# Kernel optimization log

Measured on AMD Instinct MI355X. Metric: run time of the kernel, lower is better.

Reference implementation:

```python
import jax, jax.numpy as jnp
import numpy as np

N_NODES = 20000
N_EDGES = 50000
IN_DIM = 128
HID = 128
OUT_DIM = 64
N_PAIRS = 128
N_LAYERS = 2
N_HEADS = 4


def setup_inputs() -> dict:
    key = jax.random.key(0)
    ks = jax.random.split(key, 32)
    s = 0.05
    def p(k, shape):
        return jax.random.normal(k, shape, jnp.float32) * s
    inp = {}
    inp["node_features"] = jax.random.normal(ks[0], (N_NODES, IN_DIM), jnp.float32)
    inp["edge_index"] = jax.random.randint(ks[1], (2, N_EDGES), 0, N_NODES, jnp.int32)
    inp["edge_timestamps"] = jax.random.uniform(ks[2], (N_EDGES,), jnp.float32)
    inp["target_pairs"] = jax.random.randint(ks[3], (N_PAIRS, 2), 0, N_NODES, jnp.int32)
    inp["in_W"] = p(ks[4], (HID, IN_DIM)); inp["in_b"] = p(ks[5], (HID,))
    inp["te_W1"] = p(ks[6], (N_LAYERS, HID, 1)); inp["te_b1"] = p(ks[7], (N_LAYERS, HID))
    inp["te_W2"] = p(ks[8], (N_LAYERS, HID, HID)); inp["te_b2"] = p(ks[9], (N_LAYERS, HID))
    inp["attn_in_W"] = p(ks[10], (N_LAYERS, 3 * HID, HID)); inp["attn_in_b"] = p(ks[11], (N_LAYERS, 3 * HID))
    inp["attn_out_W"] = p(ks[12], (N_LAYERS, HID, HID)); inp["attn_out_b"] = p(ks[13], (N_LAYERS, HID))
    inp["ft_W"] = p(ks[14], (N_LAYERS, HID, HID)); inp["ft_b"] = p(ks[15], (N_LAYERS, HID))
    inp["op_W"] = p(ks[16], (N_LAYERS, HID, HID)); inp["op_b"] = p(ks[17], (N_LAYERS, HID))
    inp["out1_W"] = p(ks[18], (HID, HID)); inp["out1_b"] = p(ks[19], (HID,))
    inp["out2_W"] = p(ks[20], (OUT_DIM, HID)); inp["out2_b"] = p(ks[21], (OUT_DIM,))
    inp["lp1_W"] = p(ks[22], (HID, 2 * OUT_DIM)); inp["lp1_b"] = p(ks[23], (HID,))
    inp["lp2_W"] = p(ks[24], (HID // 2, HID)); inp["lp2_b"] = p(ks[25], (HID // 2,))
    inp["lp3_W"] = p(ks[26], (1, HID // 2)); inp["lp3_b"] = p(ks[27], (1,))
    return inp


def _forward(node_features, edge_index, edge_timestamps, target_pairs,
             in_W, in_b, te_W1, te_b1, te_W2, te_b2,
             attn_in_W, attn_in_b, attn_out_W, attn_out_b,
             ft_W, ft_b, op_W, op_b,
             out1_W, out1_b, out2_W, out2_b,
             lp1_W, lp1_b, lp2_W, lp2_b, lp3_W, lp3_b):
    N = node_features.shape[0]
    h = in_W.shape[0]
    H = N_HEADS
    d = h // H
    scale = 1.0 / np.sqrt(d).astype(np.float32)
    src, dst = edge_index[0], edge_index[1]
    # flattened target nodes; duplicates compute identical rows so dedup (torch.unique) is unneeded
    targets = target_pairs.reshape(-1)  # [U]
    U = targets.shape[0]
    E = src.shape[0]

    x = node_features @ in_W.T + in_b  # [N, h]
    for l in range(te_W1.shape[0]):
        tf = x @ ft_W[l].T + ft_b[l]                                           # [N, h]
        tfeat = jax.nn.relu(edge_timestamps[:, None] @ te_W1[l].T + te_b1[l])
        tfeat = tfeat @ te_W2[l].T + te_b2[l]                                  # [E, h]
        Wq, Wk, Wv = jnp.split(attn_in_W[l], 3, axis=0)
        bq, bk, bv = jnp.split(attn_in_b[l], 3)
        q = (tf[targets] @ Wq.T + bq).reshape(U, H, d)
        # keys/values are linear in (tf[nbr] + tfeat): split into node term A and edge term B
        Ak = (tf @ Wk.T).reshape(N, H, d)
        Bk = (tfeat @ Wk.T + bk).reshape(E, H, d)
        Av = (tf @ Wv.T).reshape(N, H, d)
        Bv = (tfeat @ Wv.T + bv).reshape(E, H, d)
        is_src = src[None, :] == targets[:, None]          # [U, E]
        mask = is_src | (dst[None, :] == targets[:, None])  # edge incident to target
        nbr = jnp.where(is_src, dst[None, :], src[None, :])  # other endpoint, [U, E]
        qAk = jnp.einsum('uhd,nhd->uhn', q, Ak) * scale      # [U, H, N]
        idx = jnp.broadcast_to(nbr[:, None, :], (U, H, E))
        s_node = jnp.take_along_axis(qAk, idx, axis=2)        # [U, H, E]
        s_edge = jnp.einsum('uhd,ehd->uhe', q, Bk) * scale
        scores = jnp.where(mask[:, None, :], s_node + s_edge, -1e30)
        p = jax.nn.softmax(scores, axis=-1)
        p = jnp.where(mask[:, None, :], p, 0.0)               # [U, H, E]
        out_edge = jnp.einsum('uhe,ehd->uhd', p, Bv)
        # sum_e p * Av[nbr] via per-target scatter of probs into node space
        w = jax.vmap(lambda pe, ne: jax.ops.segment_sum(pe, ne, num_segments=N))(
            p.transpose(0, 2, 1), nbr)                        # [U, N, H]
        out_node = jnp.einsum('unh,nhd->uhd', w, Av)
        attn = (out_node + out_edge).reshape(U, h) @ attn_out_W[l].T + attn_out_b[l]
        has_nbr = mask.any(axis=1)
        agg_in = jnp.where(has_nbr[:, None], attn, tf[targets])
        agg = agg_in @ op_W[l].T + op_b[l]
        x = x.at[targets].set(agg)
        x = jax.nn.relu(x)
    emb = jax.nn.relu(x @ out1_W.T + out1_b) @ out2_W.T + out2_b  # [N, out]
    pair = jnp.concatenate([emb[target_pairs[:, 0]], emb[target_pairs[:, 1]]], axis=1)
    z = jax.nn.relu(pair @ lp1_W.T + lp1_b)
    z = jax.nn.relu(z @ lp2_W.T + lp2_b)
    return jax.nn.sigmoid(z @ lp3_W.T + lp3_b)  # [B, 1]


def reference(node_features, edge_index, edge_timestamps, target_pairs,
              in_W, in_b, te_W1, te_b1, te_W2, te_b2,
              attn_in_W, attn_in_b, attn_out_W, attn_out_b,
              ft_W, ft_b, op_W, op_b,
              out1_W, out1_b, out2_W, out2_b,
              lp1_W, lp1_b, lp2_W, lp2_b, lp3_W, lp3_b):
    return _forward(node_features, edge_index, edge_timestamps, target_pairs,
                    in_W, in_b, te_W1, te_b1, te_W2, te_b2,
                    attn_in_W, attn_in_b, attn_out_W, attn_out_b,
                    ft_W, ft_b, op_W, op_b,
                    out1_W, out1_b, out2_W, out2_b,
                    lp1_W, lp1_b, lp2_W, lp2_b, lp3_W, lp3_b)
```

## Files before the change

kernel.cpp:

```cpp
#include <hip/hip_runtime.h>
#include <math.h>

#define N_NODES 20000
#define N_EDGES 50000
#define N_SLOTS 256
#define N_PAIRS 128
#define CAP 64
#define MSTRIDE 16384
#define NMAT 19
#define TFLAG (1 << 30)

__device__ __forceinline__ float4 relu4(float4 v) {
    return make_float4(fmaxf(v.x, 0.f), fmaxf(v.y, 0.f), fmaxf(v.z, 0.f), fmaxf(v.w, 0.f));
}
__device__ __forceinline__ float4 add4(float4 a, float4 b) {
    return make_float4(a.x + b.x, a.y + b.y, a.z + b.z, a.w + b.w);
}
__device__ __forceinline__ void fma4(float4& acc, const float4 w, const float s) {
    acc.x = fmaf(w.x, s, acc.x); acc.y = fmaf(w.y, s, acc.y);
    acc.z = fmaf(w.z, s, acc.z); acc.w = fmaf(w.w, s, acc.w);
}
#define F4Z make_float4(0.f, 0.f, 0.f, 0.f)

__device__ __forceinline__ float4 mv_ks1_g8(const float* __restrict__ WT,
                                            const float* __restrict__ xv128,
                                            int g, int jj) {
    const float4* W4 = (const float4*)WT;
    const float4* x4 = (const float4*)xv128;
    float4 acc = F4Z;
#pragma unroll
    for (int kk4 = 0; kk4 < 4; ++kk4) {
        int k4 = g * 4 + kk4;
        float4 xv = x4[k4];
        fma4(acc, W4[(k4 * 4 + 0) * 32 + jj], xv.x);
        fma4(acc, W4[(k4 * 4 + 1) * 32 + jj], xv.y);
        fma4(acc, W4[(k4 * 4 + 2) * 32 + jj], xv.z);
        fma4(acc, W4[(k4 * 4 + 3) * 32 + jj], xv.w);
    }
    return acc;
}
__device__ __forceinline__ float4 mv_ks1_g8_64(const float* __restrict__ WT,
                                               const float* __restrict__ xv128,
                                               int g, int jj) {
    const float4* W4 = (const float4*)WT;
    const float4* x4 = (const float4*)xv128;
    int j16 = jj & 15;
    float4 acc = F4Z;
#pragma unroll
    for (int kk4 = 0; kk4 < 4; ++kk4) {
        int k4 = g * 4 + kk4;
        float4 xv = x4[k4];
        fma4(acc, W4[(k4 * 4 + 0) * 16 + j16], xv.x);
        fma4(acc, W4[(k4 * 4 + 1) * 16 + j16], xv.y);
        fma4(acc, W4[(k4 * 4 + 2) * 16 + j16], xv.z);
        fma4(acc, W4[(k4 * 4 + 3) * 16 + j16], xv.w);
    }
    return acc;
}
__device__ __forceinline__ void mv8_g8(const float* __restrict__ WT,
                                       const float* __restrict__ xs,
                                       int g, int jj, float4* acc) {
    const float4* W4 = (const float4*)WT;
    const float4* x4 = (const float4*)xs;
#pragma unroll
    for (int kk4 = 0; kk4 < 4; ++kk4) {
        int k4 = g * 4 + kk4;
        float4 w0 = W4[(k4 * 4 + 0) * 32 + jj];
        float4 w1 = W4[(k4 * 4 + 1) * 32 + jj];
        float4 w2 = W4[(k4 * 4 + 2) * 32 + jj];
        float4 w3 = W4[(k4 * 4 + 3) * 32 + jj];
#pragma unroll
        for (int e = 0; e < 8; ++e) {
            float4 xv = x4[e * 32 + k4];
            fma4(acc[e], w0, xv.x); fma4(acc[e], w1, xv.y);
            fma4(acc[e], w2, xv.z); fma4(acc[e], w3, xv.w);
        }
    }
}
__device__ __forceinline__ float4 comb1_g8(const float4* pb, int jj) {
    float4 s = pb[jj];
#pragma unroll
    for (int gp = 1; gp < 8; ++gp) s = add4(s, pb[gp * 32 + jj]);
    return s;
}
__device__ __forceinline__ float4 comb8_g8(const float4* pb, int it, int jj) {
    float4 s = pb[it * 32 + jj];
#pragma unroll
    for (int gp = 1; gp < 8; ++gp) s = add4(s, pb[(gp * 8 + it) * 32 + jj]);
    return s;
}

__device__ __forceinline__ float4 mv_ks1(const float* __restrict__ WT,
                                         const float* __restrict__ xv128,
                                         int g, int jj) {
    const float4* W4 = (const float4*)WT;
    const float4* x4 = (const float4*)xv128;
    float4 acc = F4Z;
#pragma unroll 2
    for (int kk4 = 0; kk4 < 8; ++kk4) {
        int k4 = g * 8 + kk4;
        float4 xv = x4[k4];
        fma4(acc, W4[(k4 * 4 + 0) * 32 + jj], xv.x);
        fma4(acc, W4[(k4 * 4 + 1) * 32 + jj], xv.y);
        fma4(acc, W4[(k4 * 4 + 2) * 32 + jj], xv.z);
        fma4(acc, W4[(k4 * 4 + 3) * 32 + jj], xv.w);
    }
    return acc;
}
__device__ __forceinline__ float4 mv_ks1_64(const float* __restrict__ WT,
                                            const float* __restrict__ xv128,
                                            int g, int jj) {
    const float4* W4 = (const float4*)WT;
    const float4* x4 = (const float4*)xv128;
    int j16 = jj & 15;
    float4 acc = F4Z;
#pragma unroll 2
    for (int kk4 = 0; kk4 < 8; ++kk4) {
        int k4 = g * 8 + kk4;
        float4 xv = x4[k4];
        fma4(acc, W4[(k4 * 4 + 0) * 16 + j16], xv.x);
        fma4(acc, W4[(k4 * 4 + 1) * 16 + j16], xv.y);
        fma4(acc, W4[(k4 * 4 + 2) * 16 + j16], xv.z);
        fma4(acc, W4[(k4 * 4 + 3) * 16 + j16], xv.w);
    }
    return acc;
}
__device__ __forceinline__ float4 comb1(const float4* pb, int jj) {
    return add4(add4(pb[jj], pb[32 + jj]), add4(pb[64 + jj], pb[96 + jj]));
}


__global__ __launch_bounds__(256) void k_prep_tr(
    const int* __restrict__ ei, const int* __restrict__ tp,
    const float* __restrict__ inW, const float* __restrict__ ftW,
    const float* __restrict__ teW2, const float* __restrict__ aiW,
    const float* __restrict__ aoW, const float* __restrict__ opW,
    const float* __restrict__ o1W, const float* __restrict__ o2W,
    const float* __restrict__ l1W, const float* __restrict__ l2W,
    float* __restrict__ WT, int* __restrict__ cnt, int2* __restrict__ lst) {
    __shared__ float tile[32][129];
    __shared__ int tps[N_SLOTS];
    __shared__ int lc;
    const int b = blockIdx.x;
    if (threadIdx.x == 0) lc = 0;
    if (b < 72) {
        int m, r0, rows;
        if (b < 68) { m = b >> 2; r0 = (b & 3) * 32; rows = 128; }
        else { int mm = b - 68; m = 17 + (mm >> 1); r0 = (mm & 1) * 32; rows = 64; }
        const float* src;
        if (m == 0) src = inW;
        else if (m <= 2) src = ftW + (m - 1) * MSTRIDE;
        else if (m <= 4) src = teW2 + (m - 3) * MSTRIDE;
        else if (m <= 10) src = aiW + (m - 5) * MSTRIDE;
        else if (m <= 12) src = aoW + (m - 11) * MSTRIDE;
        else if (m <= 14) src = opW + (m - 13) * MSTRIDE;
        else if (m == 15) src = o1W;
        else if (m == 16) src = l1W;
        else if (m == 17) src = o2W;
        else src = l2W;
        float* dst = WT + m * MSTRIDE;
        for (int idx = threadIdx.x; idx < 32 * 128; idx += 256) {
            int r = idx >> 7, c = idx & 127;
            tile[r][c] = src[(r0 + r) * 128 + c];
        }
        __syncthreads();
        for (int idx = threadIdx.x; idx < 128 * 32; idx += 256) {
            int k = idx >> 5, jr = idx & 31;
            dst[k * rows + r0 + jr] = tile[jr][k];
        }
    }
    for (int i = threadIdx.x; i < N_SLOTS; i += 256) tps[i] = tp[i];
    __syncthreads();
    const int u = tps[b];
    const int4* src4 = (const int4*)ei;
    const int4* dst4 = (const int4*)(ei + N_EDGES);
    for (int e4 = threadIdx.x; e4 < N_EDGES / 4; e4 += 256) {
        int4 s = src4[e4];
        int4 d = dst4[e4];
        int ss[4] = {s.x, s.y, s.z, s.w};
        int dd[4] = {d.x, d.y, d.z, d.w};
#pragma unroll
        for (int t = 0; t < 4; ++t) {
            if (ss[t] == u || dd[t] == u) {
                int nbr = (ss[t] == u) ? dd[t] : ss[t];
                int pos = atomicAdd(&lc, 1);
                if (pos < CAP) lst[b * CAP + pos] = make_int2(e4 * 4 + t, nbr);
            }
        }
    }
    __syncthreads();
    if (threadIdx.x == 0) cnt[b] = lc;
    int c = min(lc, CAP);
    if (threadIdx.x < c) {
        int2 en = lst[b * CAP + threadIdx.x];
        bool ist = false;
        for (int t = 0; t < N_SLOTS; ++t) ist |= (tps[t] == en.y);
        if (ist) { en.y |= TFLAG; lst[b * CAP + threadIdx.x] = en; }
    }
}

__global__ __launch_bounds__(256) void k_layer(
    const float* __restrict__ nf, const float* __restrict__ x,
    const float* __restrict__ ts, const int* __restrict__ tp,
    const int* __restrict__ cnt, const int2* __restrict__ lst,
    const float* __restrict__ WT_in, const float* __restrict__ inb,
    const float* __restrict__ WT_ft, const float* __restrict__ ftb,
    const float* __restrict__ teW1, const float* __restrict__ teb1,
    const float* __restrict__ WT_te2, const float* __restrict__ teb2,
    const float* __restrict__ WT_q, const float* __restrict__ bq,
    const float* __restrict__ WT_k, const float* __restrict__ bk,
    const float* __restrict__ WT_v, const float* __restrict__ bv,
    const float* __restrict__ WT_ao, const float* __restrict__ aob,
    const float* __restrict__ WT_op, const float* __restrict__ opb,
    const float* __restrict__ WT_o1, const float* __restrict__ o1b,
    const float* __restrict__ WT_o2, const float* __restrict__ o2b,
    float* __restrict__ x_out, float* __restrict__ emb, int layer) {
    __shared__ __align__(16) float xu[128], x0u[128], tfv[128], qv[128], sv[128];
    __shared__ __align__(16) float xs[8 * 128], t1s[8 * 128], x0s[8 * 128], zs[8 * 128];
    __shared__ __align__(16) float4 pb[8 * 8 * 32];
    __shared__ __align__(16) float vbl[CAP * 128];
    __shared__ float scl[CAP * 4];
    __shared__ int nbr_s[8], tf_s[8];
    __shared__ float ts_s[8];
    const int slot = blockIdx.x, tid = threadIdx.x, g = tid >> 5, jj = tid & 31;
    const float scale = 0.17677669529663687f;
    const int u = tp[slot];
    const int c = min(cnt[slot], CAP);

    if (tid < 128) xu[tid] = (layer == 0) ? nf[(size_t)u * 128 + tid]
                                          : x[(size_t)u * 128 + tid];
    __syncthreads();
    const float* xeff = xu;
    if (layer == 0) {
        pb[g * 32 + jj] = mv_ks1_g8(WT_in, xu, g, jj);
        __syncthreads();
        if (g == 0)
            *(float4*)(x0u + jj * 4) = add4(comb1_g8(pb, jj), *(const float4*)(inb + jj * 4));
        xeff = x0u;
        __syncthreads();
    }
    pb[g * 32 + jj] = mv_ks1_g8(WT_ft, xeff, g, jj);
    __syncthreads();
    if (g == 0)
        *(float4*)(tfv + jj * 4) = add4(comb1_g8(pb, jj), *(const float4*)(ftb + jj * 4));
    __syncthreads();
    pb[g * 32 + jj] = mv_ks1_g8(WT_q, tfv, g, jj);
    __syncthreads();
    if (g == 0)
        *(float4*)(qv + jj * 4) = add4(comb1_g8(pb, jj), *(const float4*)(bq + jj * 4));
    __syncthreads();

    for (int base = 0; base < c; base += 8) {
        if (tid < 8) {
            int i = base + tid;
            int2 en = (i < c) ? lst[slot * CAP + i] : make_int2(0, 0);
            nbr_s[tid] = en.y & ~TFLAG;
            tf_s[tid] = (en.y & TFLAG) ? 1 : 0;
            ts_s[tid] = (i < c) ? ts[en.x] : 0.f;
        }
        __syncthreads();
        {
            int e = tid >> 5, c0 = jj * 4;
            const float* srcp = (layer == 0) ? (nf + (size_t)nbr_s[e] * 128 + c0)
                                             : (x + (size_t)nbr_s[e] * 128 + c0);
            float4 v = *(const float4*)srcp;
            float* dstp = (layer == 0) ? xs : x0s;
            *(float4*)(dstp + e * 128 + c0) = v;
            float tse = ts_s[e];
            float4 w = *(const float4*)(teW1 + c0);
            float4 b = *(const float4*)(teb1 + c0);
            *(float4*)(t1s + e * 128 + c0) =
                make_float4(fmaxf(fmaf(tse, w.x, b.x), 0.f),
                            fmaxf(fmaf(tse, w.y, b.y), 0.f),
                            fmaxf(fmaf(tse, w.z, b.z), 0.f),
                            fmaxf(fmaf(tse, w.w, b.w), 0.f));
        }
        __syncthreads();
        if (layer == 0) {
            float4 acc[8] = {F4Z, F4Z, F4Z, F4Z, F4Z, F4Z, F4Z, F4Z};
            mv8_g8(WT_in, xs, g, jj, acc);
#pragma unroll
            for (int e = 0; e < 8; ++e) pb[(g * 8 + e) * 32 + jj] = acc[e];
            __syncthreads();
            {
                float4 x0v = add4(comb8_g8(pb, g, jj), *(const float4*)(inb + jj * 4));
                *(float4*)(x0s + g * 128 + jj * 4) = x0v;
                if (base + g < c && !tf_s[g])
                    *(float4*)(x_out + (size_t)nbr_s[g] * 128 + jj * 4) = relu4(x0v);
            }
            __syncthreads();
        }
        {
            float4 acc[8] = {F4Z, F4Z, F4Z, F4Z, F4Z, F4Z, F4Z, F4Z};
            mv8_g8(WT_ft, x0s, g, jj, acc);
#pragma unroll
            for (int e = 0; e < 8; ++e) pb[(g * 8 + e) * 32 + jj] = acc[e];
            __syncthreads();
            float4 za = comb8_g8(pb, g, jj);
            __syncthreads();
            float4 acc2[8] = {F4Z, F4Z, F4Z, F4Z, F4Z, F4Z, F4Z, F4Z};
            mv8_g8(WT_te2, t1s, g, jj, acc2);
#pragma unroll
            for (int e = 0; e < 8; ++e) pb[(g * 8 + e) * 32 + jj] = acc2[e];
            __syncthreads();
            float4 zb = comb8_g8(pb, g, jj);
            float4 z4 = add4(add4(za, zb),
                             add4(*(const float4*)(ftb + jj * 4),
                                  *(const float4*)(teb2 + jj * 4)));
            *(float4*)(zs + g * 128 + jj * 4) = z4;
            __syncthreads();
        }
        {
            float4 acc[8] = {F4Z, F4Z, F4Z, F4Z, F4Z, F4Z, F4Z, F4Z};
            mv8_g8(WT_k, zs, g, jj, acc);
#pragma unroll
            for (int e = 0; e < 8; ++e) pb[(g * 8 + e) * 32 + jj] = acc[e];
            __syncthreads();
            float4 kk = add4(comb8_g8(pb, g, jj), *(const float4*)(bk + jj * 4));
            __syncthreads();
            float4 acc2[8] = {F4Z, F4Z, F4Z, F4Z, F4Z, F4Z, F4Z, F4Z};
            mv8_g8(WT_v, zs, g, jj, acc2);
#pragma unroll
            for (int e = 0; e < 8; ++e) pb[(g * 8 + e) * 32 + jj] = acc2[e];
            __syncthreads();
            float4 vv = add4(comb8_g8(pb, g, jj), *(const float4*)(bv + jj * 4));
            float4 q4 = *(const float4*)(qv + jj * 4);
            float pr = q4.x * kk.x + q4.y * kk.y + q4.z * kk.z + q4.w * kk.w;
            pr += __shfl_xor(pr, 1);
            pr += __shfl_xor(pr, 2);
            pr += __shfl_xor(pr, 4);
            if (base + g < c) {
                if ((jj & 7) == 0) scl[(base + g) * 4 + (jj >> 3)] = pr * scale;
                *(float4*)(vbl + (base + g) * 128 + jj * 4) = vv;
            }
            __syncthreads();
        }
    }

    if (tid < 128) {
        int h = tid >> 5;
        if (c > 0) {
            float m = -INFINITY;
            for (int i = 0; i < c; ++i) m = fmaxf(m, scl[i * 4 + h]);
            float l = 0.f, o = 0.f;
            for (int i = 0; i < c; ++i) {
                float p = __expf(scl[i * 4 + h] - m);
                l += p;
                o = fmaf(p, vbl[i * 128 + tid], o);
            }
            sv[tid] = o / l;
        } else {
            sv[tid] = 0.f;
        }
    }
    __syncthreads();
    pb[g * 32 + jj] = mv_ks1_g8(WT_ao, sv, g, jj);
    __syncthreads();
    if (g == 0) {
        float4 z4;
        if (c > 0) z4 = add4(comb1_g8(pb, jj), *(const float4*)(aob + jj * 4));
        else z4 = *(const float4*)(tfv + jj * 4);
        *(float4*)(xu + jj * 4) = z4;
    }
    __syncthreads();
    pb[g * 32 + jj] = mv_ks1_g8(WT_op, xu, g, jj);
    __syncthreads();
    if (layer == 0) {
        if (g == 0) {
            float4 a = relu4(add4(comb1_g8(pb, jj), *(const float4*)(opb + jj * 4)));
            *(float4*)(x_out + (size_t)u * 128 + jj * 4) = a;
        }
        return;
    }
    if (g == 0)
        *(float4*)(x0u + jj * 4) =
            relu4(add4(comb1_g8(pb, jj), *(const float4*)(opb + jj * 4)));
    __syncthreads();
    pb[g * 32 + jj] = mv_ks1_g8(WT_o1, x0u, g, jj);
    __syncthreads();
    if (g == 0)
        *(float4*)(tfv + jj * 4) =
            relu4(add4(comb1_g8(pb, jj), *(const float4*)(o1b + jj * 4)));
    __syncthreads();
    pb[g * 32 + jj] = mv_ks1_g8_64(WT_o2, tfv, g, jj);
    __syncthreads();
    if (g == 0 && jj < 16)
        *(float4*)(emb + (size_t)slot * 64 + jj * 4) =
            add4(comb1_g8(pb, jj), *(const float4*)(o2b + jj * 4));
}

__global__ __launch_bounds__(128) void k_pair(
    const float* __restrict__ emb,
    const float* __restrict__ WT_l1, const float* __restrict__ l1b,
    const float* __restrict__ WT_l2, const float* __restrict__ l2b,
    const float* __restrict__ l3W, const float* __restrict__ l3b,
    float* __restrict__ out) {
    __shared__ __align__(16) float pv[128], z1[128], z2s[64];
    __shared__ __align__(16) float4 pb[4 * 32];
    const int p = blockIdx.x, tid = threadIdx.x, g = tid >> 5, jj = tid & 31;
    pv[tid] = (tid < 64) ? emb[(size_t)(2 * p) * 64 + tid]
                         : emb[(size_t)(2 * p + 1) * 64 + (tid - 64)];
    __syncthreads();
    pb[g * 32 + jj] = mv_ks1(WT_l1, pv, g, jj);
    __syncthreads();
    if (g == 0)
        *(float4*)(z1 + jj * 4) = relu4(add4(comb1(pb, jj), *(const float4*)(l1b + jj * 4)));
    __syncthreads();
    pb[g * 32 + jj] = mv_ks1_64(WT_l2, z1, g, jj);
    __syncthreads();
    if (g == 0 && jj < 16)
        *(float4*)(z2s + jj * 4) = relu4(add4(comb1(pb, jj), *(const float4*)(l2b + jj * 4)));
    __syncthreads();
    if (tid < 64) {
        float v = z2s[tid] * l3W[tid];
        v += __shfl_xor(v, 1);
        v += __shfl_xor(v, 2);
        v += __shfl_xor(v, 4);
        v += __shfl_xor(v, 8);
        v += __shfl_xor(v, 16);
        v += __shfl_xor(v, 32);
        if (tid == 0) out[p] = 1.f / (1.f + __expf(-(v + l3b[0])));
    }
}

extern "C" void kernel_launch(void* const* d_in, const int* in_sizes, int n_in,
                              void* d_out, int out_size, void* d_ws, size_t ws_size,
                              hipStream_t stream) {
    const float* nf  = (const float*)d_in[0];
    const int*   ei  = (const int*)d_in[1];
    const float* ts  = (const float*)d_in[2];
    const int*   tp  = (const int*)d_in[3];
    const float* inW = (const float*)d_in[4];
    const float* inb = (const float*)d_in[5];
    const float* teW1 = (const float*)d_in[6];
    const float* teb1 = (const float*)d_in[7];
    const float* teW2 = (const float*)d_in[8];
    const float* teb2 = (const float*)d_in[9];
    const float* aiW = (const float*)d_in[10];
    const float* aib = (const float*)d_in[11];
    const float* aoW = (const float*)d_in[12];
    const float* aob = (const float*)d_in[13];
    const float* ftW = (const float*)d_in[14];
    const float* ftb = (const float*)d_in[15];
    const float* opW = (const float*)d_in[16];
    const float* opb = (const float*)d_in[17];
    const float* o1W = (const float*)d_in[18];
    const float* o1b = (const float*)d_in[19];
    const float* o2W = (const float*)d_in[20];
    const float* o2b = (const float*)d_in[21];
    const float* l1W = (const float*)d_in[22];
    const float* l1b = (const float*)d_in[23];
    const float* l2W = (const float*)d_in[24];
    const float* l2b = (const float*)d_in[25];
    const float* l3W = (const float*)d_in[26];
    const float* l3b = (const float*)d_in[27];
    float* out = (float*)d_out;

    char* ws = (char*)d_ws;
    size_t off = 0;
    float* x    = (float*)(ws + off); off += (size_t)N_NODES * 128 * 4;
    int*   cnt  = (int*)  (ws + off); off += N_SLOTS * 4;
    int2*  lst  = (int2*) (ws + off); off += (size_t)N_SLOTS * CAP * 8;
    float* emb  = (float*)(ws + off); off += N_SLOTS * 64 * 4;
    float* WT   = (float*)(ws + off); off += (size_t)NMAT * MSTRIDE * 4;

    k_prep_tr<<<N_SLOTS, 256, 0, stream>>>(ei, tp, inW, ftW, teW2, aiW, aoW, opW,
                                           o1W, o2W, l1W, l2W, WT, cnt, lst);

    for (int l = 0; l < 2; ++l) {
        const float* WT_ft = WT + (1 + l) * MSTRIDE;
        const float* WT_te2 = WT + (3 + l) * MSTRIDE;
        const float* WT_q = WT + (5 + 3 * l) * MSTRIDE;
        const float* WT_k = WT + (6 + 3 * l) * MSTRIDE;
        const float* WT_v = WT + (7 + 3 * l) * MSTRIDE;
        const float* WT_ao = WT + (11 + l) * MSTRIDE;
        const float* WT_op = WT + (13 + l) * MSTRIDE;
        const float* bq = aib + l * 384;
        k_layer<<<N_SLOTS, 256, 0, stream>>>(
            nf, x, ts, tp, cnt, lst,
            WT, inb, WT_ft, ftb + l * 128, teW1 + l * 128, teb1 + l * 128,
            WT_te2, teb2 + l * 128, WT_q, bq, WT_k, bq + 128, WT_v, bq + 256,
            WT_ao, aob + l * 128, WT_op, opb + l * 128,
            WT + 15 * MSTRIDE, o1b, WT + 17 * MSTRIDE, o2b,
            x, emb, l);
    }
    k_pair<<<N_PAIRS, 128, 0, stream>>>(emb, WT + 16 * MSTRIDE, l1b,
                                        WT + 18 * MSTRIDE, l2b, l3W, l3b, out);
}
```

Measured before the change: 200.9 us.

## Precompose Q/K/V with feature-transform weights and fuse pair head into last layer

Precomputes products of the attention Q/K/V projection matrices with the feature-transform and time-encoding weights, plus folded biases, in the prep kernel. The layer kernel then goes from input to q, k and v in one matvec stage, and the K and V matvecs share a single barrier. The separate pair-MLP kernel is removed: the second block of each pair finishes it, detected through an atomic counter and threadfence. This cuts sequential matvec stages, barriers and one launch, at the cost of more prep work, doubled shared staging, and different float rounding from reassociation.

```diff
diff --git a/kernel.cpp b/kernel.cpp
--- a/kernel.cpp
+++ b/kernel.cpp
@@ -8,6 +8,7 @@
 #define CAP 64
 #define MSTRIDE 16384
 #define NMAT 19
+#define NPROD 10
 #define TFLAG (1 << 30)
 
 __device__ __forceinline__ float4 relu4(float4 v) {
@@ -90,59 +91,29 @@
     return s;
 }
 
-__device__ __forceinline__ float4 mv_ks1(const float* __restrict__ WT,
-                                         const float* __restrict__ xv128,
-                                         int g, int jj) {
-    const float4* W4 = (const float4*)WT;
-    const float4* x4 = (const float4*)xv128;
-    float4 acc = F4Z;
-#pragma unroll 2
-    for (int kk4 = 0; kk4 < 8; ++kk4) {
-        int k4 = g * 8 + kk4;
-        float4 xv = x4[k4];
-        fma4(acc, W4[(k4 * 4 + 0) * 32 + jj], xv.x);
-        fma4(acc, W4[(k4 * 4 + 1) * 32 + jj], xv.y);
-        fma4(acc, W4[(k4 * 4 + 2) * 32 + jj], xv.z);
-        fma4(acc, W4[(k4 * 4 + 3) * 32 + jj], xv.w);
-    }
-    return acc;
-}
-__device__ __forceinline__ float4 mv_ks1_64(const float* __restrict__ WT,
-                                            const float* __restrict__ xv128,
-                                            int g, int jj) {
-    const float4* W4 = (const float4*)WT;
-    const float4* x4 = (const float4*)xv128;
-    int j16 = jj & 15;
-    float4 acc = F4Z;
-#pragma unroll 2
-    for (int kk4 = 0; kk4 < 8; ++kk4) {
-        int k4 = g * 8 + kk4;
-        float4 xv = x4[k4];
-        fma4(acc, W4[(k4 * 4 + 0) * 16 + j16], xv.x);
-        fma4(acc, W4[(k4 * 4 + 1) * 16 + j16], xv.y);
-        fma4(acc, W4[(k4 * 4 + 2) * 16 + j16], xv.z);
-        fma4(acc, W4[(k4 * 4 + 3) * 16 + j16], xv.w);
-    }
-    return acc;
-}
-__device__ __forceinline__ float4 comb1(const float4* pb, int jj) {
-    return add4(add4(pb[jj], pb[32 + jj]), add4(pb[64 + jj], pb[96 + jj]));
-}
-
 
 __global__ __launch_bounds__(256) void k_prep_tr(
     const int* __restrict__ ei, const int* __restrict__ tp,
     const float* __restrict__ inW, const float* __restrict__ ftW,
     const float* __restrict__ teW2, const float* __restrict__ aiW,
+    const float* __restrict__ aib,
     const float* __restrict__ aoW, const float* __restrict__ opW,
     const float* __restrict__ o1W, const float* __restrict__ o2W,
     const float* __restrict__ l1W, const float* __restrict__ l2W,
-    float* __restrict__ WT, int* __restrict__ cnt, int2* __restrict__ lst) {
+    const float* __restrict__ ftb, const float* __restrict__ teb2,
+    float* __restrict__ WT, float* __restrict__ WP, float* __restrict__ WB,
+    int* __restrict__ pairflag,
+    int* __restrict__ cnt, int2* __restrict__ lst) {
     __shared__ float tile[32][129];
+    __shared__ __align__(16) float As[128 * 128];
+    __shared__ __align__(16) float Bs[128 * 16];
+    __shared__ float bv_s[128];
     __shared__ int tps[N_SLOTS];
     __shared__ int lc;
     const int b = blockIdx.x;
-    if (threadIdx.x == 0) lc = 0;
+    const int tid = threadIdx.x;
+    if (tid == 0) lc = 0;
+    if (b == 0 && tid < N_PAIRS) pairflag[tid] = 0;
     if (b < 72) {
         int m, r0, rows;
         if (b < 68) { m = b >> 2; r0 = (b & 3) * 32; rows = 128; }
@@ -159,43 +130,100 @@
         else if (m == 17) src = o2W;
         else src = l2W;
         float* dst = WT + m * MSTRIDE;
-        for (int idx = threadIdx.x; idx < 32 * 128; idx += 256) {
+        for (int idx = tid; idx < 32 * 128; idx += 256) {
             int r = idx >> 7, c = idx & 127;
             tile[r][c] = src[(r0 + r) * 128 + c];
         }
         __syncthreads();
-        for (int idx = threadIdx.x; idx < 128 * 32; idx += 256) {
+        for (int idx = tid; idx < 128 * 32; idx += 256) {
             int k = idx >> 5, jr = idx & 31;
             dst[k * rows + r0 + jr] = tile[jr][k];
         }
-    }
-    for (int i = threadIdx.x; i < N_SLOTS; i += 256) tps[i] = tp[i];
+    } else if (b < 152) {
+        const int pidx = (b - 72) >> 3, mseg = (b - 72) & 7, m0 = mseg * 16;
+        const int l = pidx / 5, t = pidx % 5;
+        const float* A = aiW + l * 3 * MSTRIDE +
+                         ((t == 0) ? 0 : (t <= 2) ? MSTRIDE : 2 * MSTRIDE);
+        const float* B = ((t == 2 || t == 4) ? teW2 : ftW) + l * MSTRIDE;
+        {
+            const float4* A4 = (const float4*)A;
+            float4* As4 = (float4*)As;
+            for (int idx = tid; idx < 4096; idx += 256) As4[idx] = A4[idx];
+            for (int idx = tid; idx < 2048; idx += 256) {
+                int j = idx >> 4, mm = idx & 15;
+                Bs[idx] = B[j * 128 + m0 + mm];
+            }
+            if (tid < 128) {
+                float bb = ftb[l * 128 + tid];
+                if (t != 0) bb += teb2[l * 128 + tid];
+                bv_s[tid] = bb;
+            }
+        }
+        __syncthreads();
+        {
+            const int i = tid & 127, half = tid >> 7;
+            const float4* As4 = (const float4*)As;
+            const float4* Bs4 = (const float4*)Bs;
+            float4 accA = F4Z, accB = F4Z;
+#pragma unroll 4
+            for (int j4 = 0; j4 < 32; ++j4) {
+                float4 a4 = As4[i * 32 + j4];
+#pragma unroll
+                for (int jo = 0; jo < 4; ++jo) {
+                    int j = j4 * 4 + jo;
+                    float aj = (jo == 0) ? a4.x : (jo == 1) ? a4.y : (jo == 2) ? a4.z : a4.w;
+                    float4 b0 = Bs4[j * 4 + half * 2 + 0];
+                    float4 b1 = Bs4[j * 4 + half * 2 + 1];
+                    fma4(accA, b0, aj);
+                    fma4(accB, b1, aj);
+                }
+            }
+            float* dst = WP + pidx * MSTRIDE;
+            float o[8] = {accA.x, accA.y, accA.z, accA.w, accB.x, accB.y, accB.z, accB.w};
+#pragma unroll
+            for (int r = 0; r < 8; ++r) dst[(m0 + half * 8 + r) * 128 + i] = o[r];
+        }
+        if (mseg == 0 && (t == 0 || t == 1 || t == 3) && tid < 128) {
+            const float4* As4 = (const float4*)As;
+            const float4* bs4 = (const float4*)bv_s;
+            float acc = 0.f;
+#pragma unroll 4
+            for (int j4 = 0; j4 < 32; ++j4) {
+                float4 a4 = As4[tid * 32 + j4];
+                float4 b4 = bs4[j4];
+                acc = fmaf(a4.x, b4.x, fmaf(a4.y, b4.y, fmaf(a4.z, b4.z, fmaf(a4.w, b4.w, acc))));
+            }
+            int which = (t == 0) ? 0 : (t == 1) ? 1 : 2;
+            WB[l * 384 + which * 128 + tid] = acc + aib[l * 384 + which * 128 + tid];
+        }
+    }
+    for (int i = tid; i < N_SLOTS; i += 256) tps[i] = tp[i];
     __syncthreads();
     const int u = tps[b];
     const int4* src4 = (const int4*)ei;
     const int4* dst4 = (const int4*)(ei + N_EDGES);
-    for (int e4 = threadIdx.x; e4 < N_EDGES / 4; e4 += 256) {
+    for (int e4 = tid; e4 < N_EDGES / 4; e4 += 256) {
         int4 s = src4[e4];
         int4 d = dst4[e4];
         int ss[4] = {s.x, s.y, s.z, s.w};
         int dd[4] = {d.x, d.y, d.z, d.w};
 #pragma unroll
-        for (int t = 0; t < 4; ++t) {
-            if (ss[t] == u || dd[t] == u) {
-                int nbr = (ss[t] == u) ? dd[t] : ss[t];
+        for (int t2 = 0; t2 < 4; ++t2) {
+            if (ss[t2] == u || dd[t2] == u) {
+                int nbr = (ss[t2] == u) ? dd[t2] : ss[t2];
                 int pos = atomicAdd(&lc, 1);
-                if (pos < CAP) lst[b * CAP + pos] = make_int2(e4 * 4 + t, nbr);
-            }
-        }
-    }
-    __syncthreads();
-    if (threadIdx.x == 0) cnt[b] = lc;
+                if (pos < CAP) lst[b * CAP + pos] = make_int2(e4 * 4 + t2, nbr);
+            }
+        }
+    }
+    __syncthreads();
+    if (tid == 0) cnt[b] = lc;
     int c = min(lc, CAP);
-    if (threadIdx.x < c) {
-        int2 en = lst[b * CAP + threadIdx.x];
+    if (tid < c) {
+        int2 en = lst[b * CAP + tid];
         bool ist = false;
-        for (int t = 0; t < N_SLOTS; ++t) ist |= (tps[t] == en.y);
-        if (ist) { en.y |= TFLAG; lst[b * CAP + threadIdx.x] = en; }
+        for (int t2 = 0; t2 < N_SLOTS; ++t2) ist |= (tps[t2] == en.y);
+        if (ist) { en.y |= TFLAG; lst[b * CAP + tid] = en; }
     }
 }
 
@@ -206,26 +234,33 @@
     const float* __restrict__ WT_in, const float* __restrict__ inb,
     const float* __restrict__ WT_ft, const float* __restrict__ ftb,
     const float* __restrict__ teW1, const float* __restrict__ teb1,
-    const float* __restrict__ WT_te2, const float* __restrict__ teb2,
-    const float* __restrict__ WT_q, const float* __restrict__ bq,
-    const float* __restrict__ WT_k, const float* __restrict__ bk,
-    const float* __restrict__ WT_v, const float* __restrict__ bv,
+    const float* __restrict__ WPq, const float* __restrict__ WkF,
+    const float* __restrict__ WkT, const float* __restrict__ WvF,
+    const float* __restrict__ WvT, const float* __restrict__ WBl,
     const float* __restrict__ WT_ao, const float* __restrict__ aob,
     const float* __restrict__ WT_op, const float* __restrict__ opb,
     const float* __restrict__ WT_o1, const float* __restrict__ o1b,
     const float* __restrict__ WT_o2, const float* __restrict__ o2b,
-    float* __restrict__ x_out, float* __restrict__ emb, int layer) {
+    const float* __restrict__ WT_l1, const float* __restrict__ l1b,
+    const float* __restrict__ WT_l2, const float* __restrict__ l2b,
+    const float* __restrict__ l3W, const float* __restrict__ l3b,
+    float* __restrict__ x_out, float* __restrict__ emb,
+    int* __restrict__ pairflag, float* __restrict__ out, int layer) {
     __shared__ __align__(16) float xu[128], x0u[128], tfv[128], qv[128], sv[128];
-    __shared__ __align__(16) float xs[8 * 128], t1s[8 * 128], x0s[8 * 128], zs[8 * 128];
-    __shared__ __align__(16) float4 pb[8 * 8 * 32];
+    __shared__ __align__(16) float xs[8 * 128], t1s[8 * 128], x0s[8 * 128];
+    __shared__ __align__(16) float4 pb[2 * 8 * 8 * 32];
     __shared__ __align__(16) float vbl[CAP * 128];
     __shared__ float scl[CAP * 4];
     __shared__ int nbr_s[8], tf_s[8];
     __shared__ float ts_s[8];
+    __shared__ int win_s;
     const int slot = blockIdx.x, tid = threadIdx.x, g = tid >> 5, jj = tid & 31;
     const float scale = 0.17677669529663687f;
     const int u = tp[slot];
     const int c = min(cnt[slot], CAP);
+    const float* bqp = WBl;
+    const float* bkp = WBl + 128;
+    const float* bvp = WBl + 256;
 
     if (tid < 128) xu[tid] = (layer == 0) ? nf[(size_t)u * 128 + tid]
                                           : x[(size_t)u * 128 + tid];
@@ -240,14 +275,12 @@
         __syncthreads();
     }
     pb[g * 32 + jj] = mv_ks1_g8(WT_ft, xeff, g, jj);
-    __syncthreads();
-    if (g == 0)
+    pb[2048 + g * 32 + jj] = mv_ks1_g8(WPq, xeff, g, jj);
+    __syncthreads();
+    if (g == 0) {
         *(float4*)(tfv + jj * 4) = add4(comb1_g8(pb, jj), *(const float4*)(ftb + jj * 4));
-    __syncthreads();
-    pb[g * 32 + jj] = mv_ks1_g8(WT_q, tfv, g, jj);
-    __syncthreads();
-    if (g == 0)
-        *(float4*)(qv + jj * 4) = add4(comb1_g8(pb, jj), *(const float4*)(bq + jj * 4));
+        *(float4*)(qv + jj * 4) = add4(comb1_g8(pb + 2048, jj), *(const float4*)(bqp + jj * 4));
+    }
     __syncthreads();
 
     for (int base = 0; base < c; base += 8) {
@@ -292,38 +325,18 @@
         }
         {
             float4 acc[8] = {F4Z, F4Z, F4Z, F4Z, F4Z, F4Z, F4Z, F4Z};
-            mv8_g8(WT_ft, x0s, g, jj, acc);
+            mv8_g8(WkF, x0s, g, jj, acc);
+            mv8_g8(WkT, t1s, g, jj, acc);
 #pragma unroll
             for (int e = 0; e < 8; ++e) pb[(g * 8 + e) * 32 + jj] = acc[e];
+            float4 acc2[8] = {F4Z, F4Z, F4Z, F4Z, F4Z, F4Z, F4Z, F4Z};
+            mv8_g8(WvF, x0s, g, jj, acc2);
+            mv8_g8(WvT, t1s, g, jj, acc2);
+#pragma unroll
+            for (int e = 0; e < 8; ++e) pb[2048 + (g * 8 + e) * 32 + jj] = acc2[e];
             __syncthreads();
-            float4 za = comb8_g8(pb, g, jj);
-            __syncthreads();
-            float4 acc2[8] = {F4Z, F4Z, F4Z, F4Z, F4Z, F4Z, F4Z, F4Z};
-            mv8_g8(WT_te2, t1s, g, jj, acc2);
-#pragma unroll
-            for (int e = 0; e < 8; ++e) pb[(g * 8 + e) * 32 + jj] = acc2[e];
-            __syncthreads();
-            float4 zb = comb8_g8(pb, g, jj);
-            float4 z4 = add4(add4(za, zb),
-                             add4(*(const float4*)(ftb + jj * 4),
-                                  *(const float4*)(teb2 + jj * 4)));
-            *(float4*)(zs + g * 128 + jj * 4) = z4;
-            __syncthreads();
-        }
-        {
-            float4 acc[8] = {F4Z, F4Z, F4Z, F4Z, F4Z, F4Z, F4Z, F4Z};
-            mv8_g8(WT_k, zs, g, jj, acc);
-#pragma unroll
-            for (int e = 0; e < 8; ++e) pb[(g * 8 + e) * 32 + jj] = acc[e];
-            __syncthreads();
-            float4 kk = add4(comb8_g8(pb, g, jj), *(const float4*)(bk + jj * 4));
-            __syncthreads();
-            float4 acc2[8] = {F4Z, F4Z, F4Z, F4Z, F4Z, F4Z, F4Z, F4Z};
-            mv8_g8(WT_v, zs, g, jj, acc2);
-#pragma unroll
-            for (int e = 0; e < 8; ++e) pb[(g * 8 + e) * 32 + jj] = acc2[e];
-            __syncthreads();
-            float4 vv = add4(comb8_g8(pb, g, jj), *(const float4*)(bv + jj * 4));
+            float4 kk = add4(comb8_g8(pb, g, jj), *(const float4*)(bkp + jj * 4));
+            float4 vv = add4(comb8_g8(pb + 2048, g, jj), *(const float4*)(bvp + jj * 4));
             float4 q4 = *(const float4*)(qv + jj * 4);
             float pr = q4.x * kk.x + q4.y * kk.y + q4.z * kk.z + q4.w * kk.w;
             pr += __shfl_xor(pr, 1);
@@ -384,35 +397,33 @@
     __syncthreads();
     pb[g * 32 + jj] = mv_ks1_g8_64(WT_o2, tfv, g, jj);
     __syncthreads();
-    if (g == 0 && jj < 16)
+    if (g == 0 && jj < 16) {
         *(float4*)(emb + (size_t)slot * 64 + jj * 4) =
             add4(comb1_g8(pb, jj), *(const float4*)(o2b + jj * 4));
-}
-
-__global__ __launch_bounds__(128) void k_pair(
-    const float* __restrict__ emb,
-    const float* __restrict__ WT_l1, const float* __restrict__ l1b,
-    const float* __restrict__ WT_l2, const float* __restrict__ l2b,
-    const float* __restrict__ l3W, const float* __restrict__ l3b,
-    float* __restrict__ out) {
-    __shared__ __align__(16) float pv[128], z1[128], z2s[64];
-    __shared__ __align__(16) float4 pb[4 * 32];
-    const int p = blockIdx.x, tid = threadIdx.x, g = tid >> 5, jj = tid & 31;
-    pv[tid] = (tid < 64) ? emb[(size_t)(2 * p) * 64 + tid]
-                         : emb[(size_t)(2 * p + 1) * 64 + (tid - 64)];
-    __syncthreads();
-    pb[g * 32 + jj] = mv_ks1(WT_l1, pv, g, jj);
+        __threadfence();
+    }
+    __syncthreads();
+    if (tid == 0) win_s = atomicAdd(&pairflag[slot >> 1], 1);
+    __syncthreads();
+    if (win_s == 0) return;
+    __threadfence();
+    const int p = slot >> 1;
+    if (tid < 128)
+        sv[tid] = (tid < 64) ? emb[(size_t)(2 * p) * 64 + tid]
+                             : emb[(size_t)(2 * p + 1) * 64 + (tid - 64)];
+    __syncthreads();
+    pb[g * 32 + jj] = mv_ks1_g8(WT_l1, sv, g, jj);
     __syncthreads();
     if (g == 0)
-        *(float4*)(z1 + jj * 4) = relu4(add4(comb1(pb, jj), *(const float4*)(l1b + jj * 4)));
-    __syncthreads();
-    pb[g * 32 + jj] = mv_ks1_64(WT_l2, z1, g, jj);
+        *(float4*)(xu + jj * 4) = relu4(add4(comb1_g8(pb, jj), *(const float4*)(l1b + jj * 4)));
+    __syncthreads();
+    pb[g * 32 + jj] = mv_ks1_g8_64(WT_l2, xu, g, jj);
     __syncthreads();
     if (g == 0 && jj < 16)
-        *(float4*)(z2s + jj * 4) = relu4(add4(comb1(pb, jj), *(const float4*)(l2b + jj * 4)));
+        *(float4*)(x0u + jj * 4) = relu4(add4(comb1_g8(pb, jj), *(const float4*)(l2b + jj * 4)));
     __syncthreads();
     if (tid < 64) {
-        float v = z2s[tid] * l3W[tid];
+        float v = x0u[tid] * l3W[tid];
         v += __shfl_xor(v, 1);
         v += __shfl_xor(v, 2);
         v += __shfl_xor(v, 4);
@@ -462,28 +473,31 @@
     int*   cnt  = (int*)  (ws + off); off += N_SLOTS * 4;
     int2*  lst  = (int2*) (ws + off); off += (size_t)N_SLOTS * CAP * 8;
     float* emb  = (float*)(ws + off); off += N_SLOTS * 64 * 4;
+    int*   pfl  = (int*)  (ws + off); off += N_PAIRS * 4;
     float* WT   = (float*)(ws + off); off += (size_t)NMAT * MSTRIDE * 4;
-
-    k_prep_tr<<<N_SLOTS, 256, 0, stream>>>(ei, tp, inW, ftW, teW2, aiW, aoW, opW,
-                                           o1W, o2W, l1W, l2W, WT, cnt, lst);
+    float* WP   = (float*)(ws + off); off += (size_t)NPROD * MSTRIDE * 4;
+    float* WB   = (float*)(ws + off); off += 2 * 384 * 4;
+
+    k_prep_tr<<<N_SLOTS, 256, 0, stream>>>(ei, tp, inW, ftW, teW2, aiW, aib,
+                                           aoW, opW, o1W, o2W, l1W, l2W,
+                                           ftb, teb2, WT, WP, WB, pfl, cnt, lst);
 
     for (int l = 0; l < 2; ++l) {
         const float* WT_ft = WT + (1 + l) * MSTRIDE;
-        const float* WT_te2 = WT + (3 + l) * MSTRIDE;
-        const float* WT_q = WT + (5 + 3 * l) * MSTRIDE;
-        const float* WT_k = WT + (6 + 3 * l) * MSTRIDE;
-        const float* WT_v = WT + (7 + 3 * l) * MSTRIDE;
+        const float* WPq = WP + (l * 5 + 0) * MSTRIDE;
+        const float* WkF = WP + (l * 5 + 1) * MSTRIDE;
+        const float* WkT = WP + (l * 5 + 2) * MSTRIDE;
+        const float* WvF = WP + (l * 5 + 3) * MSTRIDE;
+        const float* WvT = WP + (l * 5 + 4) * MSTRIDE;
         const float* WT_ao = WT + (11 + l) * MSTRIDE;
         const float* WT_op = WT + (13 + l) * MSTRIDE;
-        const float* bq = aib + l * 384;
         k_layer<<<N_SLOTS, 256, 0, stream>>>(
             nf, x, ts, tp, cnt, lst,
             WT, inb, WT_ft, ftb + l * 128, teW1 + l * 128, teb1 + l * 128,
-            WT_te2, teb2 + l * 128, WT_q, bq, WT_k, bq + 128, WT_v, bq + 256,
+            WPq, WkF, WkT, WvF, WvT, WB + l * 384,
             WT_ao, aob + l * 128, WT_op, opb + l * 128,
             WT + 15 * MSTRIDE, o1b, WT + 17 * MSTRIDE, o2b,
-            x, emb, l);
-    }
-    k_pair<<<N_PAIRS, 128, 0, stream>>>(emb, WT + 16 * MSTRIDE, l1b,
-                                        WT + 18 * MSTRIDE, l2b, l3W, l3b, out);
-}
+            WT + 16 * MSTRIDE, l1b, WT + 18 * MSTRIDE, l2b, l3W, l3b,
+            x, emb, pfl, out, l);
+    }
+}
```

New measurement: 345.9 us. 72.2% more time.

## Fuse pair-prediction MLP into final layer kernel via last-arriver atomic flag

Applied to the files above, without the earlier changes.

Drops the separate k_pair launch. Each block of the last layer publishes its embedding, bumps a per-pair atomic counter, and the second block of each pair to arrive runs the link-prediction MLP with the 8-group matvec helpers. This removes one kernel launch and its dependency gap. In exchange it adds threadfences and an atomic to every layer block, and relies on correct memory ordering for cross-block emb visibility.

```diff
diff --git a/kernel.cpp b/kernel.cpp
--- a/kernel.cpp
+++ b/kernel.cpp
@@ -90,45 +90,6 @@
     return s;
 }
 
-__device__ __forceinline__ float4 mv_ks1(const float* __restrict__ WT,
-                                         const float* __restrict__ xv128,
-                                         int g, int jj) {
-    const float4* W4 = (const float4*)WT;
-    const float4* x4 = (const float4*)xv128;
-    float4 acc = F4Z;
-#pragma unroll 2
-    for (int kk4 = 0; kk4 < 8; ++kk4) {
-        int k4 = g * 8 + kk4;
-        float4 xv = x4[k4];
-        fma4(acc, W4[(k4 * 4 + 0) * 32 + jj], xv.x);
-        fma4(acc, W4[(k4 * 4 + 1) * 32 + jj], xv.y);
-        fma4(acc, W4[(k4 * 4 + 2) * 32 + jj], xv.z);
-        fma4(acc, W4[(k4 * 4 + 3) * 32 + jj], xv.w);
-    }
-    return acc;
-}
-__device__ __forceinline__ float4 mv_ks1_64(const float* __restrict__ WT,
-                                            const float* __restrict__ xv128,
-                                            int g, int jj) {
-    const float4* W4 = (const float4*)WT;
-    const float4* x4 = (const float4*)xv128;
-    int j16 = jj & 15;
-    float4 acc = F4Z;
-#pragma unroll 2
-    for (int kk4 = 0; kk4 < 8; ++kk4) {
-        int k4 = g * 8 + kk4;
-        float4 xv = x4[k4];
-        fma4(acc, W4[(k4 * 4 + 0) * 16 + j16], xv.x);
-        fma4(acc, W4[(k4 * 4 + 1) * 16 + j16], xv.y);
-        fma4(acc, W4[(k4 * 4 + 2) * 16 + j16], xv.z);
-        fma4(acc, W4[(k4 * 4 + 3) * 16 + j16], xv.w);
-    }
-    return acc;
-}
-__device__ __forceinline__ float4 comb1(const float4* pb, int jj) {
-    return add4(add4(pb[jj], pb[32 + jj]), add4(pb[64 + jj], pb[96 + jj]));
-}
-
 
 __global__ __launch_bounds__(256) void k_prep_tr(
     const int* __restrict__ ei, const int* __restrict__ tp,
@@ -137,12 +98,14 @@
     const float* __restrict__ aoW, const float* __restrict__ opW,
     const float* __restrict__ o1W, const float* __restrict__ o2W,
     const float* __restrict__ l1W, const float* __restrict__ l2W,
-    float* __restrict__ WT, int* __restrict__ cnt, int2* __restrict__ lst) {
+    float* __restrict__ WT, int* __restrict__ pairflag,
+    int* __restrict__ cnt, int2* __restrict__ lst) {
     __shared__ float tile[32][129];
     __shared__ int tps[N_SLOTS];
     __shared__ int lc;
     const int b = blockIdx.x;
     if (threadIdx.x == 0) lc = 0;
+    if (b == 0 && threadIdx.x < N_PAIRS) pairflag[threadIdx.x] = 0;
     if (b < 72) {
         int m, r0, rows;
         if (b < 68) { m = b >> 2; r0 = (b & 3) * 32; rows = 128; }
@@ -214,7 +177,11 @@
     const float* __restrict__ WT_op, const float* __restrict__ opb,
     const float* __restrict__ WT_o1, const float* __restrict__ o1b,
     const float* __restrict__ WT_o2, const float* __restrict__ o2b,
-    float* __restrict__ x_out, float* __restrict__ emb, int layer) {
+    const float* __restrict__ WT_l1, const float* __restrict__ l1b,
+    const float* __restrict__ WT_l2, const float* __restrict__ l2b,
+    const float* __restrict__ l3W, const float* __restrict__ l3b,
+    float* __restrict__ x_out, float* __restrict__ emb,
+    int* __restrict__ pairflag, float* __restrict__ out, int layer) {
     __shared__ __align__(16) float xu[128], x0u[128], tfv[128], qv[128], sv[128];
     __shared__ __align__(16) float xs[8 * 128], t1s[8 * 128], x0s[8 * 128], zs[8 * 128];
     __shared__ __align__(16) float4 pb[8 * 8 * 32];
@@ -222,6 +189,7 @@
     __shared__ float scl[CAP * 4];
     __shared__ int nbr_s[8], tf_s[8];
     __shared__ float ts_s[8];
+    __shared__ int win_s;
     const int slot = blockIdx.x, tid = threadIdx.x, g = tid >> 5, jj = tid & 31;
     const float scale = 0.17677669529663687f;
     const int u = tp[slot];
@@ -384,35 +352,33 @@
     __syncthreads();
     pb[g * 32 + jj] = mv_ks1_g8_64(WT_o2, tfv, g, jj);
     __syncthreads();
-    if (g == 0 && jj < 16)
+    if (g == 0 && jj < 16) {
         *(float4*)(emb + (size_t)slot * 64 + jj * 4) =
             add4(comb1_g8(pb, jj), *(const float4*)(o2b + jj * 4));
-}
-
-__global__ __launch_bounds__(128) void k_pair(
-    const float* __restrict__ emb,
-    const float* __restrict__ WT_l1, const float* __restrict__ l1b,
-    const float* __restrict__ WT_l2, const float* __restrict__ l2b,
-    const float* __restrict__ l3W, const float* __restrict__ l3b,
-    float* __restrict__ out) {
-    __shared__ __align__(16) float pv[128], z1[128], z2s[64];
-    __shared__ __align__(16) float4 pb[4 * 32];
-    const int p = blockIdx.x, tid = threadIdx.x, g = tid >> 5, jj = tid & 31;
-    pv[tid] = (tid < 64) ? emb[(size_t)(2 * p) * 64 + tid]
-                         : emb[(size_t)(2 * p + 1) * 64 + (tid - 64)];
-    __syncthreads();
-    pb[g * 32 + jj] = mv_ks1(WT_l1, pv, g, jj);
+        __threadfence();
+    }
+    __syncthreads();
+    if (tid == 0) win_s = atomicAdd(&pairflag[slot >> 1], 1);
+    __syncthreads();
+    if (win_s == 0) return;
+    __threadfence();
+    const int p = slot >> 1;
+    if (tid < 128)
+        sv[tid] = (tid < 64) ? emb[(size_t)(2 * p) * 64 + tid]
+                             : emb[(size_t)(2 * p + 1) * 64 + (tid - 64)];
+    __syncthreads();
+    pb[g * 32 + jj] = mv_ks1_g8(WT_l1, sv, g, jj);
     __syncthreads();
     if (g == 0)
-        *(float4*)(z1 + jj * 4) = relu4(add4(comb1(pb, jj), *(const float4*)(l1b + jj * 4)));
-    __syncthreads();
-    pb[g * 32 + jj] = mv_ks1_64(WT_l2, z1, g, jj);
+        *(float4*)(xu + jj * 4) = relu4(add4(comb1_g8(pb, jj), *(const float4*)(l1b + jj * 4)));
+    __syncthreads();
+    pb[g * 32 + jj] = mv_ks1_g8_64(WT_l2, xu, g, jj);
     __syncthreads();
     if (g == 0 && jj < 16)
-        *(float4*)(z2s + jj * 4) = relu4(add4(comb1(pb, jj), *(const float4*)(l2b + jj * 4)));
+        *(float4*)(x0u + jj * 4) = relu4(add4(comb1_g8(pb, jj), *(const float4*)(l2b + jj * 4)));
     __syncthreads();
     if (tid < 64) {
-        float v = z2s[tid] * l3W[tid];
+        float v = x0u[tid] * l3W[tid];
         v += __shfl_xor(v, 1);
         v += __shfl_xor(v, 2);
         v += __shfl_xor(v, 4);
@@ -462,10 +428,11 @@
     int*   cnt  = (int*)  (ws + off); off += N_SLOTS * 4;
     int2*  lst  = (int2*) (ws + off); off += (size_t)N_SLOTS * CAP * 8;
     float* emb  = (float*)(ws + off); off += N_SLOTS * 64 * 4;
+    int*   pfl  = (int*)  (ws + off); off += N_PAIRS * 4;
     float* WT   = (float*)(ws + off); off += (size_t)NMAT * MSTRIDE * 4;
 
     k_prep_tr<<<N_SLOTS, 256, 0, stream>>>(ei, tp, inW, ftW, teW2, aiW, aoW, opW,
-                                           o1W, o2W, l1W, l2W, WT, cnt, lst);
+                                           o1W, o2W, l1W, l2W, WT, pfl, cnt, lst);
 
     for (int l = 0; l < 2; ++l) {
         const float* WT_ft = WT + (1 + l) * MSTRIDE;
@@ -482,8 +449,7 @@
             WT_te2, teb2 + l * 128, WT_q, bq, WT_k, bq + 128, WT_v, bq + 256,
             WT_ao, aob + l * 128, WT_op, opb + l * 128,
             WT + 15 * MSTRIDE, o1b, WT + 17 * MSTRIDE, o2b,
-            x, emb, l);
-    }
-    k_pair<<<N_PAIRS, 128, 0, stream>>>(emb, WT + 16 * MSTRIDE, l1b,
-                                        WT + 18 * MSTRIDE, l2b, l3W, l3b, out);
-}
+            WT + 16 * MSTRIDE, l1b, WT + 18 * MSTRIDE, l2b, l3W, l3b,
+            x, emb, pfl, out, l);
+    }
+}
```

Measured after the change: 210.8 us. 4.9% more time.
